# Performance work log

Hardware: AMD Instinct MI355X
Metric: run time of the kernel (lower is better)

The kernel has to match this reference:

```python
import jax, jax.numpy as jnp
import numpy as np

FP8_MAX = 448.0  # float8_e4m3 max finite value


def setup_inputs() -> dict:
    key = jax.random.key(0)
    k1, k2, k3, k4, k5 = jax.random.split(key, 5)
    B, S, IN, OUT = 8, 2048, 2048, 2048
    x = jax.random.normal(k1, (B, S, IN), dtype=jnp.float32)
    weight = jax.random.normal(k2, (OUT, IN), dtype=jnp.float32) * 0.02
    bias = jax.random.normal(k3, (OUT,), dtype=jnp.float32)
    # per-tensor scales, kept positive and away from zero
    scale_in = jax.random.uniform(k4, (1,), dtype=jnp.float32) * 0.09 + 0.01
    scale_w = jax.random.uniform(k5, (1,), dtype=jnp.float32) * 0.09 + 0.01
    return {"x": x, "weight": weight, "bias": bias,
            "scale_in": scale_in, "scale_w": scale_w}


def _fp8_quantize(x, scale):
    # divide by scale, saturate to fp8 range, cast to fp8 e4m3
    q = jnp.clip(x / scale, -FP8_MAX, FP8_MAX)
    return q.astype(jnp.float8_e4m3fn)


def reference(x, weight, bias, scale_in, scale_w):
    # quantize input and weight to fp8 (per-tensor scales)
    xq = _fp8_quantize(x, scale_in)            # [B,S,IN] fp8
    wq = _fp8_quantize(weight, scale_w)        # [OUT,IN] fp8
    # scaled matmul: accumulate in fp32, dequant with scale_a*scale_b, emit fp16
    acc = jnp.einsum('bsk,nk->bsn', xq.astype(jnp.float32), wq.astype(jnp.float32))
    out = (acc * (scale_in[0] * scale_w[0])).astype(jnp.float16)
    out = out + bias.astype(jnp.float16)       # trailing bias add at fp16
    return out
```

## Files before the change

### kernel.cpp

```cpp
#include <hip/hip_runtime.h>
#include <hip/hip_fp16.h>
#include <stdint.h>

#define MDIM 16384
#define NDIM 2048
#define KDIM 2048

typedef __attribute__((ext_vector_type(4))) float f32x4;
typedef __attribute__((ext_vector_type(4))) int   i32x4;
typedef __attribute__((ext_vector_type(8))) int   i32x8;

#if defined(__has_builtin)
#if __has_builtin(__builtin_amdgcn_cvt_pk_fp8_f32)
#define HAVE_CVT_PK_FP8 1
#endif
#endif

__device__ __forceinline__ unsigned f32_to_e4m3(float x) {
    float q = fminf(448.f, fmaxf(-448.f, x));
    unsigned ub = __float_as_uint(q);
    unsigned sgn = (ub >> 24) & 0x80u;
    float aq = fabsf(q);
    int E = (int)((__float_as_uint(aq) >> 23) & 0xff) - 127;
    if (E < -6) E = -6;
    float rq = __uint_as_float((unsigned)(130 - E) << 23);
    int m = (int)rintf(aq * rq);
    if (m == 16) { m = 8; E += 1; }
    unsigned bits;
    if (m < 8) bits = sgn | (unsigned)m;
    else       bits = sgn | ((unsigned)(E + 7) << 3) | (unsigned)(m - 8);
    return bits;
}

__device__ __forceinline__ uint32_t pack4_e4m3(float a, float b, float c, float d) {
#ifdef HAVE_CVT_PK_FP8
    int r = __builtin_amdgcn_cvt_pk_fp8_f32(a, b, 0, false);
    r = __builtin_amdgcn_cvt_pk_fp8_f32(c, d, r, true);
    return (uint32_t)r;
#else
    return f32_to_e4m3(a) | (f32_to_e4m3(b) << 8) |
           (f32_to_e4m3(c) << 16) | (f32_to_e4m3(d) << 24);
#endif
}

__global__ void quant_both_kernel(const float* __restrict__ x,
                                  uint8_t* __restrict__ xq,
                                  const float* __restrict__ w,
                                  uint8_t* __restrict__ wq,
                                  const float* __restrict__ s_in,
                                  const float* __restrict__ s_w) {
    if (blockIdx.x < 2048) {
        float sc = s_in[0];
        unsigned n16 = (unsigned)((size_t)MDIM * KDIM / 16);
        unsigned i = blockIdx.x * 256 + threadIdx.x;
        for (; i < n16; i += 2048 * 256) {
            const float4* xp = (const float4*)(x + (size_t)i * 16);
            uint32_t wd[4];
#pragma unroll
            for (int j = 0; j < 4; ++j) {
                float4 v = xp[j];
                wd[j] = pack4_e4m3(v.x / sc, v.y / sc, v.z / sc, v.w / sc);
            }
            ((uint4*)xq)[i] = make_uint4(wd[0], wd[1], wd[2], wd[3]);
        }
    } else {
        float sc = s_w[0];
        unsigned n16 = (unsigned)((size_t)NDIM * KDIM / 16);
        unsigned i = (blockIdx.x - 2048) * 256 + threadIdx.x;
        for (; i < n16; i += 256 * 256) {
            const float4* xp = (const float4*)(w + (size_t)i * 16);
            uint32_t wd[4];
#pragma unroll
            for (int j = 0; j < 4; ++j) {
                float4 v = xp[j];
                wd[j] = pack4_e4m3(v.x / sc, v.y / sc, v.z / sc, v.w / sc);
            }
            unsigned r = i >> 7, kc = i & 127;
            unsigned idx = ((r >> 4) * 16 + (kc >> 3)) * 128 +
                           ((kc & 7) >> 1) * 32 + (r & 15) * 2 + (kc & 1);
            ((uint4*)wq)[idx] = make_uint4(wd[0], wd[1], wd[2], wd[3]);
        }
    }
}

#define BM 128
#define BN 256
#define BKB 128
#define NKT (KDIM / BKB)

__device__ __forceinline__ void gload_lds16(const uint8_t* g, uint8_t* l) {
    __builtin_amdgcn_global_load_lds(
        (const __attribute__((address_space(1))) void*)g,
        (__attribute__((address_space(3))) void*)l, 16, 0, 0);
}

__device__ __forceinline__ void barrier_raw() {
    asm volatile("" ::: "memory");
    __builtin_amdgcn_s_barrier();
    asm volatile("" ::: "memory");
}

__global__ __launch_bounds__(256, 2) void gemm_fp8_kernel(
    const uint8_t* __restrict__ Aq, const uint8_t* __restrict__ Bp,
    const float* __restrict__ bias, const float* __restrict__ s_in,
    const float* __restrict__ s_w, float* __restrict__ out) {

    extern __shared__ uint8_t lds[];

    int nwg = gridDim.x;
    int cpx = nwg >> 3;
    int bid = blockIdx.x;
    int swz = (bid & 7) * cpx + (bid >> 3);
    int tm = swz >> 3;
    int tn = swz & 7;
    int row0 = tm * BM;
    int col0 = tn * BN;

    int tid  = threadIdx.x;
    int lane = tid & 63;
    int wid  = tid >> 6;
    int wr = wid >> 1, wc = wid & 1;
    int r15 = lane & 15;
    int g   = lane >> 4;

    int perm0 = ((2 * g + r15) & 7) << 4;
    int perm1 = ((2 * g + 1 + r15) & 7) << 4;

    int ssrc[4], sdst[4];
#pragma unroll
    for (int i = 0; i < 4; ++i) {
        int p = i * 256 + tid;
        int lrow = p >> 3;
        int c = ((p & 7) - (lrow & 7)) & 7;
        ssrc[i] = lrow * KDIM + c * 16;
        sdst[i] = p * 16;
    }
    const uint8_t* Asrc = Aq + (size_t)row0 * KDIM;

#define STAGE_A(KT, BUF)                                                      \
    {                                                                         \
        _Pragma("unroll")                                                     \
        for (int j_ = 0; j_ < 4; ++j_)                                        \
            gload_lds16(Asrc + ssrc[j_] + (size_t)(KT) * BKB, (BUF) + sdst[j_]); \
    }

    const uint8_t* Bbase = Bp + (size_t)(tn * 16 + wc * 8) * 32768 + lane * 32;

#define LOAD_BF1(DST, N, KT)                                                  \
    {                                                                         \
        const uint8_t* p_ = Bbase + (size_t)(N) * 32768 + (size_t)(KT) * 2048; \
        i32x4 lo = *(const i32x4*)p_;                                         \
        i32x4 hi = *(const i32x4*)(p_ + 16);                                  \
        _Pragma("unroll")                                                     \
        for (int q_ = 0; q_ < 4; ++q_) { DST[q_] = lo[q_]; DST[4 + q_] = hi[q_]; } \
    }

#define LOAD_BF_ALL(KT)                                                       \
    LOAD_BF1(bf0, 0, KT); LOAD_BF1(bf1, 1, KT);                               \
    LOAD_BF1(bf2, 2, KT); LOAD_BF1(bf3, 3, KT);                               \
    LOAD_BF1(bf4, 4, KT); LOAD_BF1(bf5, 5, KT);                               \
    LOAD_BF1(bf6, 6, KT); LOAD_BF1(bf7, 7, KT);

    int aRow0 = wr * 64 + r15;

#define LOAD_AF1(DST, bo, M)                                                  \
    {                                                                         \
        const uint8_t* rp = lds + (bo) + (aRow0 + (M) * 16) * 128;            \
        i32x4 lo = *(const i32x4*)(rp + perm0);                               \
        i32x4 hi = *(const i32x4*)(rp + perm1);                               \
        _Pragma("unroll")                                                     \
        for (int q_ = 0; q_ < 4; ++q_) { DST[q_] = lo[q_]; DST[4 + q_] = hi[q_]; } \
    }

#define MFMA4N(BF, N)                                                         \
    __builtin_amdgcn_s_setprio(1);                                            \
    acc[0][N] = __builtin_amdgcn_mfma_scale_f32_16x16x128_f8f6f4(             \
        af0, BF, acc[0][N], 0, 0, 0, 127, 0, 127);                            \
    acc[1][N] = __builtin_amdgcn_mfma_scale_f32_16x16x128_f8f6f4(             \
        af1, BF, acc[1][N], 0, 0, 0, 127, 0, 127);                            \
    acc[2][N] = __builtin_amdgcn_mfma_scale_f32_16x16x128_f8f6f4(             \
        af2, BF, acc[2][N], 0, 0, 0, 127, 0, 127);                            \
    acc[3][N] = __builtin_amdgcn_mfma_scale_f32_16x16x128_f8f6f4(             \
        af3, BF, acc[3][N], 0, 0, 0, 127, 0, 127);                            \
    __builtin_amdgcn_s_setprio(0);

    f32x4 acc[4][8];
#pragma unroll
    for (int m = 0; m < 4; ++m)
#pragma unroll
        for (int n = 0; n < 8; ++n)
            acc[m][n] = (f32x4){0.f, 0.f, 0.f, 0.f};

    i32x8 bf0, bf1, bf2, bf3, bf4, bf5, bf6, bf7;
    i32x8 af0, af1, af2, af3;

    uint8_t* buf0 = &lds[0];
    uint8_t* buf1 = &lds[16384];

    STAGE_A(0, buf0);
    asm volatile("" ::: "memory");
    LOAD_BF_ALL(0);
    asm volatile("s_waitcnt vmcnt(16)" ::: "memory");
    barrier_raw();

#define TILE_BODY(T)                                                          \
    {                                                                         \
        const unsigned bo = ((unsigned)(T) & 1) << 14;                        \
        uint8_t* nxt_ = (((T) & 1) ? buf0 : buf1);                            \
        if ((T) + 1 < NKT) STAGE_A((T) + 1, nxt_);     \
        asm volatile("" ::: "memory");                                        \
        LOAD_AF1(af0, bo, 0); LOAD_AF1(af1, bo, 1);                           \
        LOAD_AF1(af2, bo, 2); LOAD_AF1(af3, bo, 3);                           \
        MFMA4N(bf0, 0);            \
        MFMA4N(bf1, 1);                                        \
        MFMA4N(bf2, 2);                        \
        MFMA4N(bf3, 3);                                                       \
        MFMA4N(bf4, 4);                                                       \
        MFMA4N(bf5, 5);                                                       \
        MFMA4N(bf6, 6);                                                       \
        MFMA4N(bf7, 7);                     \
        if ((T) + 1 < NKT) {                                                  \
            asm volatile("" ::: "memory");                                    \
            LOAD_BF_ALL((T) + 1);                \
            asm volatile("s_waitcnt vmcnt(16)" ::: "memory");  \
        } else {                                                              \
            asm volatile("s_waitcnt vmcnt(0)" ::: "memory");                  \
        }                                                                     \
        barrier_raw();                                                        \
    }

    for (int t = 0; t < NKT; ++t)
        TILE_BODY(t);

    float s = s_in[0] * s_w[0];
    float* slab = (float*)lds;
    __half hb[8];
#pragma unroll
    for (int n = 0; n < 8; ++n)
        hb[n] = __float2half(bias[col0 + wc * 128 + n * 16 + r15]);

#pragma unroll
    for (int q = 0; q < 4; ++q) {
        if (wr == (q >> 1)) {
            const int mbase = 2 * (q & 1);
#pragma unroll
            for (int n = 0; n < 8; ++n) {
                int colb = wc * 128 + n * 16 + r15;
#pragma unroll
                for (int mm = 0; mm < 2; ++mm) {
                    int sr = mm * 16 + g * 4;
#pragma unroll
                    for (int r = 0; r < 4; ++r) {
                        __half h = __float2half(acc[mbase + mm][n][r] * s);
                        slab[(sr + r) * 256 + colb] = __half2float(__hadd(h, hb[n]));
                    }
                }
            }
        }
        barrier_raw();
#pragma unroll
        for (int it = 0; it < 8; ++it) {
            int srow = wid * 8 + it;
            f32x4 vv = *(const f32x4*)&slab[srow * 256 + lane * 4];
            int grow = row0 + q * 32 + srow;
            *(f32x4*)&out[(size_t)grow * NDIM + col0 + lane * 4] = vv;
        }
        barrier_raw();
    }
#undef STAGE_A
#undef LOAD_BF1
#undef LOAD_BF_ALL
#undef LOAD_AF1
#undef MFMA4N
#undef TILE_BODY
}

extern "C" void kernel_launch(void* const* d_in, const int* in_sizes, int n_in,
                              void* d_out, int out_size, void* d_ws, size_t ws_size,
                              hipStream_t stream) {
    const float* x      = (const float*)d_in[0];
    const float* weight = (const float*)d_in[1];
    const float* bias   = (const float*)d_in[2];
    const float* s_in   = (const float*)d_in[3];
    const float* s_w    = (const float*)d_in[4];
    float* out          = (float*)d_out;

    uint8_t* xq = (uint8_t*)d_ws;
    uint8_t* wq = (uint8_t*)d_ws + (size_t)MDIM * KDIM;

    quant_both_kernel<<<2304, 256, 0, stream>>>(x, xq, weight, wq, s_in, s_w);

    dim3 grid((MDIM / BM) * (NDIM / BN));
    gemm_fp8_kernel<<<grid, 256, 32768, stream>>>(xq, wq, bias, s_in, s_w, out);
}
```

Measured before the change: 111.5 us.

## Give each wave private LDS A-tiles to drop per-tile block barriers

Each wave now stages only its own 64 A rows into a private, double-buffered LDS region using async global-to-LDS loads. This removes the workgroup barrier from every K iteration and prefetches A two tiles ahead. In exchange, the two waves that share A rows now load them twice, doubling A traffic into LDS. LDS per block grows to 64KB, which may lower occupancy.

```diff
diff --git a/kernel.cpp b/kernel.cpp
--- a/kernel.cpp
+++ b/kernel.cpp
@@ -126,22 +126,17 @@
     int perm0 = ((2 * g + r15) & 7) << 4;
     int perm1 = ((2 * g + 1 + r15) & 7) << 4;
 
-    int ssrc[4], sdst[4];
-#pragma unroll
-    for (int i = 0; i < 4; ++i) {
-        int p = i * 256 + tid;
-        int lrow = p >> 3;
-        int c = ((p & 7) - (lrow & 7)) & 7;
-        ssrc[i] = lrow * KDIM + c * 16;
-        sdst[i] = p * 16;
-    }
-    const uint8_t* Asrc = Aq + (size_t)row0 * KDIM;
-
-#define STAGE_A(KT, BUF)                                                      \
+    int csw = ((lane & 7) - ((lane >> 3) & 7)) & 7;
+    const uint8_t* sbase = Aq + (size_t)(row0 + wr * 64 + (lane >> 3)) * KDIM
+                              + csw * 16;
+    uint8_t* dbase = lds + wid * 16384 + lane * 16;
+
+#define STAGE_W(KT, H)                                                        \
     {                                                                         \
         _Pragma("unroll")                                                     \
-        for (int j_ = 0; j_ < 4; ++j_)                                        \
-            gload_lds16(Asrc + ssrc[j_] + (size_t)(KT) * BKB, (BUF) + sdst[j_]); \
+        for (int i_ = 0; i_ < 8; ++i_)                                        \
+            gload_lds16(sbase + (size_t)(KT) * BKB + (size_t)i_ * (8 * KDIM), \
+                        dbase + (H) * 8192 + i_ * 1024);                      \
     }
 
     const uint8_t* Bbase = Bp + (size_t)(tn * 16 + wc * 8) * 32768 + lane * 32;
@@ -161,11 +156,10 @@
     LOAD_BF1(bf4, 4, KT); LOAD_BF1(bf5, 5, KT);                               \
     LOAD_BF1(bf6, 6, KT); LOAD_BF1(bf7, 7, KT);
 
-    int aRow0 = wr * 64 + r15;
-
-#define LOAD_AF1(DST, bo, M)                                                  \
+#define LOAD_AF1(DST, H, M)                                                   \
     {                                                                         \
-        const uint8_t* rp = lds + (bo) + (aRow0 + (M) * 16) * 128;            \
+        const uint8_t* rp = lds + wid * 16384 + (H) * 8192 +                  \
+                            ((M) * 16 + r15) * 128;                           \
         i32x4 lo = *(const i32x4*)(rp + perm0);                               \
         i32x4 hi = *(const i32x4*)(rp + perm1);                               \
         _Pragma("unroll")                                                     \
@@ -194,43 +188,38 @@
     i32x8 bf0, bf1, bf2, bf3, bf4, bf5, bf6, bf7;
     i32x8 af0, af1, af2, af3;
 
-    uint8_t* buf0 = &lds[0];
-    uint8_t* buf1 = &lds[16384];
-
-    STAGE_A(0, buf0);
+    STAGE_W(0, 0);
     asm volatile("" ::: "memory");
     LOAD_BF_ALL(0);
-    asm volatile("s_waitcnt vmcnt(16)" ::: "memory");
-    barrier_raw();
-
-#define TILE_BODY(T)                                                          \
-    {                                                                         \
-        const unsigned bo = ((unsigned)(T) & 1) << 14;                        \
-        uint8_t* nxt_ = (((T) & 1) ? buf0 : buf1);                            \
-        if ((T) + 1 < NKT) STAGE_A((T) + 1, nxt_);     \
-        asm volatile("" ::: "memory");                                        \
-        LOAD_AF1(af0, bo, 0); LOAD_AF1(af1, bo, 1);                           \
-        LOAD_AF1(af2, bo, 2); LOAD_AF1(af3, bo, 3);                           \
-        MFMA4N(bf0, 0);            \
-        MFMA4N(bf1, 1);                                        \
-        MFMA4N(bf2, 2);                        \
-        MFMA4N(bf3, 3);                                                       \
-        MFMA4N(bf4, 4);                                                       \
-        MFMA4N(bf5, 5);                                                       \
-        MFMA4N(bf6, 6);                                                       \
-        MFMA4N(bf7, 7);                     \
-        if ((T) + 1 < NKT) {                                                  \
-            asm volatile("" ::: "memory");                                    \
-            LOAD_BF_ALL((T) + 1);                \
-            asm volatile("s_waitcnt vmcnt(16)" ::: "memory");  \
-        } else {                                                              \
-            asm volatile("s_waitcnt vmcnt(0)" ::: "memory");                  \
-        }                                                                     \
-        barrier_raw();                                                        \
-    }
-
-    for (int t = 0; t < NKT; ++t)
-        TILE_BODY(t);
+    asm volatile("" ::: "memory");
+    STAGE_W(1, 1);
+    asm volatile("s_waitcnt vmcnt(24)" ::: "memory");
+
+    for (int t = 0; t < NKT; ++t) {
+        const int h = t & 1;
+        LOAD_AF1(af0, h, 0); LOAD_AF1(af1, h, 1);
+        LOAD_AF1(af2, h, 2); LOAD_AF1(af3, h, 3);
+        MFMA4N(bf0, 0);
+        MFMA4N(bf1, 1);
+        MFMA4N(bf2, 2);
+        MFMA4N(bf3, 3);
+        MFMA4N(bf4, 4);
+        MFMA4N(bf5, 5);
+        MFMA4N(bf6, 6);
+        MFMA4N(bf7, 7);
+        if (t + 1 < NKT) {
+            asm volatile("" ::: "memory");
+            LOAD_BF_ALL(t + 1);
+            asm volatile("s_waitcnt vmcnt(16)" ::: "memory");
+            if (t + 2 < NKT) {
+                asm volatile("" ::: "memory");
+                STAGE_W(t + 2, h);
+            }
+        }
+    }
+    asm volatile("s_waitcnt vmcnt(0)" ::: "memory");
+
+    __syncthreads();
 
     float s = s_in[0] * s_w[0];
     float* slab = (float*)lds;
@@ -267,12 +256,11 @@
         }
         barrier_raw();
     }
-#undef STAGE_A
+#undef STAGE_W
 #undef LOAD_BF1
 #undef LOAD_BF_ALL
 #undef LOAD_AF1
 #undef MFMA4N
-#undef TILE_BODY
 }
 
 extern "C" void kernel_launch(void* const* d_in, const int* in_sizes, int n_in,
@@ -291,5 +279,5 @@
     quant_both_kernel<<<2304, 256, 0, stream>>>(x, xq, weight, wq, s_in, s_w);
 
     dim3 grid((MDIM / BM) * (NDIM / BN));
-    gemm_fp8_kernel<<<grid, 256, 32768, stream>>>(xq, wq, bias, s_in, s_w, out);
-}
+    gemm_fp8_kernel<<<grid, 256, 65536, stream>>>(xq, wq, bias, s_in, s_w, out);
+}
```

Result: slower. 135.8 us (+21.8%).
